# Kernel optimization log

Hardware: AMD Instinct MI355X
Metric: run time of the kernel (lower is better)

Reference implementation:

```python
import jax, jax.numpy as jnp
import numpy as np

N, E, F0, H = 100000, 3200000, 256, 128
TEMP = 2.0
ALPHA = 0.2  # leaky relu slope
EPS_BN = 1e-5
EPS_LN = 1e-5


def spmm(vals, row, col, X):
    # sparse [N,N] @ dense [N,D] via gather + segment_sum
    return jax.ops.segment_sum(vals[:, None] * X[col], row, num_segments=N)


def batchnorm(h, g, b):
    mu = jnp.mean(h, axis=0, keepdims=True)
    var = jnp.var(h, axis=0, keepdims=True)
    return (h - mu) * jax.lax.rsqrt(var + EPS_BN) * g + b


def layernorm(h, g, b):
    mu = jnp.mean(h, axis=-1, keepdims=True)
    var = jnp.var(h, axis=-1, keepdims=True)
    return (h - mu) * jax.lax.rsqrt(var + EPS_LN) * g + b


def setup_inputs() -> dict:
    key = jax.random.key(0)
    ks = jax.random.split(key, 32)
    x = jax.random.normal(ks[0], (N, F0), dtype=jnp.float32)
    edge_row = jax.random.randint(ks[1], (E,), 0, N)
    edge_col = jax.random.randint(ks[2], (E,), 0, N)
    adj_vals = jax.random.uniform(ks[3], (E,), dtype=jnp.float32) / 32.0  # ~normalized adj
    sf = lambda k, sh: jax.random.normal(k, sh, dtype=jnp.float32) * 0.05
    in_dim = 3 * F0 + 1
    return {
        "x": x, "edge_row": edge_row, "edge_col": edge_col, "adj_vals": adj_vals,
        # LowPassExtractor (GCN)
        "W_gc1": sf(ks[4], (F0, 2 * H)), "b_gc1": jnp.zeros((2 * H,), jnp.float32),
        "bn1_g": jnp.ones((2 * H,), jnp.float32), "bn1_b": jnp.zeros((2 * H,), jnp.float32),
        "W_gc2": sf(ks[5], (2 * H, H)), "b_gc2": jnp.zeros((H,), jnp.float32),
        "bn2_g": jnp.ones((H,), jnp.float32), "bn2_b": jnp.zeros((H,), jnp.float32),
        # Gating
        "Wg1": sf(ks[6], (in_dim, H)), "bg1": jnp.zeros((H,), jnp.float32),
        "ln_g": jnp.ones((H,), jnp.float32), "ln_b": jnp.zeros((H,), jnp.float32),
        "Wg2": sf(ks[7], (H, 2)), "bg2": jnp.zeros((2,), jnp.float32),
        # HighPassExpert
        "Wxp": sf(ks[8], (F0, H)), "bxp": jnp.zeros((H,), jnp.float32),
        "res_scale": jnp.asarray(1.0, jnp.float32),
        "rn_g": jnp.ones((H,), jnp.float32), "rn_b": jnp.zeros((H,), jnp.float32),
        "Wq": sf(ks[9], (H, H)), "Wk": sf(ks[10], (H, H)), "Wv": sf(ks[11], (H, H)),
    }


def reference(x, edge_row, edge_col, adj_vals,
              W_gc1, b_gc1, bn1_g, bn1_b, W_gc2, b_gc2, bn2_g, bn2_b,
              Wg1, bg1, ln_g, ln_b, Wg2, bg2,
              Wxp, bxp, res_scale, rn_g, rn_b, Wq, Wk, Wv):
    # ---- LowPassExtractor: two GCN layers (spmm(adj, xW)+b) with batchnorm+relu
    h1 = jax.nn.relu(batchnorm(spmm(adj_vals, edge_row, edge_col, x @ W_gc1) + b_gc1, bn1_g, bn1_b))
    low = jax.nn.relu(batchnorm(spmm(adj_vals, edge_row, edge_col, h1 @ W_gc2) + b_gc2, bn2_g, bn2_b))

    # ---- Gating: neighborhood stats via spmm
    AX = spmm(adj_vals, edge_row, edge_col, x)
    deg = jax.ops.segment_sum(adj_vals, edge_row, num_segments=N)[:, None]
    x_mean = AX / (deg + 1e-8)
    AX2 = spmm(adj_vals, edge_row, edge_col, x * x)
    var = AX2 / (deg + 1e-8) - x_mean * x_mean
    x_std = jnp.sqrt(jnp.clip(var, 0.0))
    x_cat = jnp.concatenate([x, AX - x, x_std, deg], axis=1)  # [N, 3*F0+1]
    hg = jax.nn.relu(layernorm(x_cat @ Wg1 + bg1, ln_g, ln_b))
    gate = jax.nn.softmax((hg @ Wg2 + bg2) / TEMP, axis=1)  # [N, 2]

    # ---- HighPassExpert: GAT-style sparse attention on normalized residual
    residual = layernorm(res_scale * (x @ Wxp + bxp - low), rn_g, rn_b)
    Q, K, V = residual @ Wq, residual @ Wk, residual @ Wv
    scores = jnp.sum(Q[edge_row] * K[edge_col], axis=1) / jnp.sqrt(jnp.float32(H))
    exp_s = jnp.exp(jnp.where(scores > 0, scores, ALPHA * scores))
    denom = jax.ops.segment_sum(exp_s, edge_row, num_segments=N)
    attn = exp_s / (denom[edge_row] + 1e-16)
    high = jax.ops.segment_sum(attn[:, None] * V[edge_col], edge_row, num_segments=N)

    output = gate[:, 0:1] * low + gate[:, 1:2] * high
    return output, gate, low, high
```

## Files before the change

kernel.cpp:

```cpp
#include <hip/hip_runtime.h>

#define F0 256
#define HD 128
#define NP 100352

typedef unsigned short u16;
typedef __attribute__((ext_vector_type(8))) short short8;
typedef __attribute__((ext_vector_type(4))) float f32x4;

__device__ inline float bf2f(u16 u) {
    union { unsigned int i; float f; } v; v.i = ((unsigned int)u) << 16; return v.f;
}
__device__ inline u16 f2bf(float f) {
    union { float f; unsigned int i; } v; v.f = f;
    unsigned int r = v.i + 0x7FFF + ((v.i >> 16) & 1);
    return (u16)(r >> 16);
}

#define GLOAD16(gp, lp) __builtin_amdgcn_global_load_lds( \
    (const __attribute__((address_space(1))) void*)(gp), \
    (__attribute__((address_space(3))) void*)(lp), 16, 0, 0)

__global__ void k_hist_rank(const int* __restrict__ row, int* __restrict__ counts,
                            int* __restrict__ rank, int E) {
    int e = blockIdx.x * blockDim.x + threadIdx.x;
    if (e < E) rank[e] = atomicAdd(&counts[row[e]], 1);
}

__global__ void k_scan_blk(const int* __restrict__ counts, int* __restrict__ scan_out,
                           int* __restrict__ partials, int n) {
    __shared__ int wsum[16];
    int t = threadIdx.x;
    int i = blockIdx.x * 1024 + t;
    int v = (i < n) ? counts[i] : 0;
    int lane = t & 63, w = t >> 6;
    #pragma unroll
    for (int off = 1; off < 64; off <<= 1) { int u = __shfl_up(v, off); if (lane >= off) v += u; }
    if (lane == 63) wsum[w] = v;
    __syncthreads();
    if (t < 16) {
        int s = wsum[t];
        #pragma unroll
        for (int off = 1; off < 16; off <<= 1) { int u = __shfl_up(s, off); if (t >= off) s += u; }
        wsum[t] = s;
    }
    __syncthreads();
    int add = (w > 0) ? wsum[w - 1] : 0;
    if (i < n) scan_out[i] = v + add;
    if (t == 1023) partials[blockIdx.x] = wsum[15];
}

__global__ void k_scan_part(int* partials, int nb) {
    __shared__ int ws2[2];
    int t = threadIdx.x;
    int v = (t < nb) ? partials[t] : 0;
    int lane = t & 63, w = t >> 6;
    #pragma unroll
    for (int off = 1; off < 64; off <<= 1) { int u = __shfl_up(v, off); if (lane >= off) v += u; }
    if (lane == 63) ws2[w] = v;
    __syncthreads();
    if (w == 1) v += ws2[0];
    if (t < nb) partials[t] = v;
}

__global__ void k_scan_add(int* __restrict__ row_ptr, const int* __restrict__ partials, int n) {
    int b = blockIdx.x;
    int i = b * 1024 + threadIdx.x;
    if (b == 0 && threadIdx.x == 0) row_ptr[0] = 0;
    int add = (b > 0) ? partials[b - 1] : 0;
    if (i < n) row_ptr[1 + i] += add;
}

__global__ void k_scatter_direct(const int* __restrict__ row, const int* __restrict__ ecol,
                                 const float* __restrict__ avals, const int* __restrict__ rank,
                                 const int* __restrict__ row_ptr, int2* __restrict__ cv, int E) {
    int e = blockIdx.x * blockDim.x + threadIdx.x;
    if (e >= E) return;
    int r = row[e];
    int pos = row_ptr[r] + rank[e];
    cv[pos] = make_int2(ecol[e], __float_as_int(avals[e]));
}

__global__ void k_cast_x(const float* __restrict__ x, u16* __restrict__ xb, int total4) {
    int i = blockIdx.x * blockDim.x + threadIdx.x;
    if (i >= total4) return;
    float4 v = ((const float4*)x)[i];
    ((ushort4*)xb)[i] = make_ushort4(f2bf(v.x), f2bf(v.y), f2bf(v.z), f2bf(v.w));
}

__global__ void k_prep_w(const float* __restrict__ W_gc1, const float* __restrict__ W_gc2,
                         const float* __restrict__ Wg1, const float* __restrict__ Wxp,
                         const float* __restrict__ Wq, const float* __restrict__ Wk,
                         const float* __restrict__ Wv,
                         u16* Wgc1t, u16* Wgc2t, u16* Wdt, u16* W1t, u16* W2t,
                         u16* Wxpt, u16* Wqt, u16* Wkt, u16* Wvt) {
    int z = blockIdx.z;
    int idx = blockIdx.x * 256 + threadIdx.x;
    if (z == 0) { if (idx < 65536) { int n = idx >> 8, k = idx & 255; Wgc1t[idx] = f2bf(W_gc1[k * 256 + n]); } }
    else if (z == 1) { if (idx < 32768) { int n = idx >> 8, k = idx & 255; Wgc2t[idx] = f2bf(W_gc2[k * 128 + n]); } }
    else if (z == 2) { if (idx < 32768) { int n = idx >> 8, k = idx & 255; Wdt[idx] = f2bf(Wg1[k * 128 + n] - Wg1[(k + 256) * 128 + n]); } }
    else if (z == 3) { if (idx < 32768) { int n = idx >> 8, k = idx & 255; W1t[idx] = f2bf(Wg1[(k + 256) * 128 + n]); } }
    else if (z == 4) { if (idx < 32768) { int n = idx >> 8, k = idx & 255; W2t[idx] = f2bf(Wg1[(k + 512) * 128 + n]); } }
    else if (z == 5) { if (idx < 32768) { int n = idx >> 8, k = idx & 255; Wxpt[idx] = f2bf(Wxp[k * 128 + n]); } }
    else if (z == 6) { if (idx < 16384) { int n = idx >> 7, k = idx & 127; Wqt[idx] = f2bf(Wq[k * 128 + n]); } }
    else if (z == 7) { if (idx < 16384) { int n = idx >> 7, k = idx & 127; Wkt[idx] = f2bf(Wk[k * 128 + n]); } }
    else if (z == 8) { if (idx < 16384) { int n = idx >> 7, k = idx & 127; Wvt[idx] = f2bf(Wv[k * 128 + n]); } }
}

__global__ void k_spmm_x2(const u16* __restrict__ Xb, const int* __restrict__ row_ptr,
                          const int2* __restrict__ cv,
                          u16* __restrict__ AXb, u16* __restrict__ XSTDb,
                          float* __restrict__ deg, int N) {
    int wid = blockIdx.x * 4 + (threadIdx.x >> 6);
    if (wid >= N) return;
    int lane = threadIdx.x & 63;
    float a0 = 0, a1 = 0, a2 = 0, a3 = 0;
    float q0 = 0, q1 = 0, q2 = 0, q3 = 0, d = 0;
    int s = row_ptr[wid], e = row_ptr[wid + 1];
    int j = s;
    for (; j + 7 < e; j += 8) {
        int2 cc[8]; ushort4 xb[8];
        #pragma unroll
        for (int t = 0; t < 8; ++t) cc[t] = cv[j + t];
        #pragma unroll
        for (int t = 0; t < 8; ++t) xb[t] = *(const ushort4*)(Xb + (size_t)cc[t].x * F0 + lane * 4);
        #pragma unroll
        for (int t = 0; t < 8; ++t) {
            float x0 = bf2f(xb[t].x), x1 = bf2f(xb[t].y), x2 = bf2f(xb[t].z), x3 = bf2f(xb[t].w);
            float vv = __int_as_float(cc[t].y);
            a0 += vv * x0; a1 += vv * x1; a2 += vv * x2; a3 += vv * x3;
            q0 += vv * x0 * x0; q1 += vv * x1 * x1; q2 += vv * x2 * x2; q3 += vv * x3 * x3;
            d += vv;
        }
    }
    for (; j + 3 < e; j += 4) {
        int2 cc[4]; ushort4 xb[4];
        #pragma unroll
        for (int t = 0; t < 4; ++t) cc[t] = cv[j + t];
        #pragma unroll
        for (int t = 0; t < 4; ++t) xb[t] = *(const ushort4*)(Xb + (size_t)cc[t].x * F0 + lane * 4);
        #pragma unroll
        for (int t = 0; t < 4; ++t) {
            float x0 = bf2f(xb[t].x), x1 = bf2f(xb[t].y), x2 = bf2f(xb[t].z), x3 = bf2f(xb[t].w);
            float vv = __int_as_float(cc[t].y);
            a0 += vv * x0; a1 += vv * x1; a2 += vv * x2; a3 += vv * x3;
            q0 += vv * x0 * x0; q1 += vv * x1 * x1; q2 += vv * x2 * x2; q3 += vv * x3 * x3;
            d += vv;
        }
    }
    for (; j < e; ++j) {
        int2 cc = cv[j];
        float v0 = __int_as_float(cc.y);
        ushort4 xb0 = *(const ushort4*)(Xb + (size_t)cc.x * F0 + lane * 4);
        float x0 = bf2f(xb0.x), x1 = bf2f(xb0.y), x2 = bf2f(xb0.z), x3 = bf2f(xb0.w);
        a0 += v0 * x0; a1 += v0 * x1; a2 += v0 * x2; a3 += v0 * x3;
        q0 += v0 * x0 * x0; q1 += v0 * x1 * x1; q2 += v0 * x2 * x2; q3 += v0 * x3 * x3;
        d += v0;
    }
    float inv = 1.0f / (d + 1e-8f);
    float m0 = a0 * inv, m1 = a1 * inv, m2 = a2 * inv, m3 = a3 * inv;
    float s0 = sqrtf(fmaxf(q0 * inv - m0 * m0, 0.f));
    float s1 = sqrtf(fmaxf(q1 * inv - m1 * m1, 0.f));
    float s2 = sqrtf(fmaxf(q2 * inv - m2 * m2, 0.f));
    float s3 = sqrtf(fmaxf(q3 * inv - m3 * m3, 0.f));
    *(ushort4*)(AXb + (size_t)wid * F0 + lane * 4) = make_ushort4(f2bf(a0), f2bf(a1), f2bf(a2), f2bf(a3));
    *(ushort4*)(XSTDb + (size_t)wid * F0 + lane * 4) = make_ushort4(f2bf(s0), f2bf(s1), f2bf(s2), f2bf(s3));
    if (lane == 0) deg[wid] = d;
}

__global__ void k_spmm128(const u16* __restrict__ Xb, const int* __restrict__ row_ptr,
                          const int2* __restrict__ cv, u16* __restrict__ OUT, int N) {
    int wid = blockIdx.x * 4 + (threadIdx.x >> 6);
    if (wid >= N) return;
    int lane = threadIdx.x & 63;
    float a0 = 0, a1 = 0;
    int s = row_ptr[wid], e = row_ptr[wid + 1];
    int j = s;
    for (; j + 7 < e; j += 8) {
        int2 cc[8]; ushort2 xb[8];
        #pragma unroll
        for (int t = 0; t < 8; ++t) cc[t] = cv[j + t];
        #pragma unroll
        for (int t = 0; t < 8; ++t) xb[t] = *(const ushort2*)(Xb + (size_t)cc[t].x * HD + lane * 2);
        #pragma unroll
        for (int t = 0; t < 8; ++t) {
            float vv = __int_as_float(cc[t].y);
            a0 += vv * bf2f(xb[t].x); a1 += vv * bf2f(xb[t].y);
        }
    }
    for (; j + 3 < e; j += 4) {
        int2 cc[4]; ushort2 xb[4];
        #pragma unroll
        for (int t = 0; t < 4; ++t) cc[t] = cv[j + t];
        #pragma unroll
        for (int t = 0; t < 4; ++t) xb[t] = *(const ushort2*)(Xb + (size_t)cc[t].x * HD + lane * 2);
        #pragma unroll
        for (int t = 0; t < 4; ++t) {
            float vv = __int_as_float(cc[t].y);
            a0 += vv * bf2f(xb[t].x); a1 += vv * bf2f(xb[t].y);
        }
    }
    for (; j < e; ++j) {
        int2 cc = cv[j];
        float v0 = __int_as_float(cc.y);
        ushort2 x0 = *(const ushort2*)(Xb + (size_t)cc.x * HD + lane * 2);
        a0 += v0 * bf2f(x0.x); a1 += v0 * bf2f(x0.y);
    }
    *(ushort2*)(OUT + (size_t)wid * HD + lane * 2) = make_ushort2(f2bf(a0), f2bf(a1));
}

__device__ inline void mm_core(const u16* __restrict__ A, const u16* __restrict__ Bt,
                               int K, int ldA, int ldB, int m0, int n0,
                               u16* As, u16* Bs, f32x4 acc[4][4]) {
    int t = threadIdx.x, w = t >> 6, l = t & 63;
    int wr = (w >> 1) * 64, wc = (w & 1) * 64;
    int aoff = (wr + (l & 15)) * 32 + (l >> 4) * 8;
    int boff = (wc + (l & 15)) * 32 + (l >> 4) * 8;
    for (int k0 = 0; k0 < K; k0 += 32) {
        __syncthreads();
        #pragma unroll
        for (int s = 0; s < 2; ++s) {
            int i = s * 256 + t;
            int row = i >> 2, ch = i & 3;
            GLOAD16(A + (size_t)(m0 + row) * ldA + k0 + ch * 8, As + i * 8);
            GLOAD16(Bt + (size_t)(n0 + row) * ldB + k0 + ch * 8, Bs + i * 8);
        }
        __syncthreads();
        short8 af[4], bfr[4];
        #pragma unroll
        for (int i = 0; i < 4; ++i) af[i] = *(const short8*)(As + aoff + i * 16 * 32);
        #pragma unroll
        for (int j = 0; j < 4; ++j) bfr[j] = *(const short8*)(Bs + boff + j * 16 * 32);
        #pragma unroll
        for (int i = 0; i < 4; ++i)
            #pragma unroll
            for (int j = 0; j < 4; ++j)
                acc[i][j] = __builtin_amdgcn_mfma_f32_16x16x32_bf16(af[i], bfr[j], acc[i][j], 0, 0, 0);
    }
}

__device__ inline void mm_zero(f32x4 acc[4][4]) {
    #pragma unroll
    for (int i = 0; i < 4; ++i)
        #pragma unroll
        for (int j = 0; j < 4; ++j)
            acc[i][j] = (f32x4){0.f, 0.f, 0.f, 0.f};
}

__global__ __launch_bounds__(256) void k_mm_f32(const u16* __restrict__ A, const u16* __restrict__ Bt,
                                                float* __restrict__ C, const float* __restrict__ bias,
                                                int M, int K, int Nc) {
    __shared__ __align__(16) u16 As[128 * 32];
    __shared__ __align__(16) u16 Bs[128 * 32];
    int m0 = blockIdx.x * 128, n0 = blockIdx.y * 128;
    f32x4 acc[4][4]; mm_zero(acc);
    mm_core(A, Bt, K, K, K, m0, n0, As, Bs, acc);
    int t = threadIdx.x, w = t >> 6, l = t & 63;
    int rbase = m0 + (w >> 1) * 64 + (l >> 4) * 4;
    int cbase = n0 + (w & 1) * 64 + (l & 15);
    #pragma unroll
    for (int j = 0; j < 4; ++j) {
        float bj = bias ? bias[cbase + j * 16] : 0.f;
        #pragma unroll
        for (int i = 0; i < 4; ++i)
            #pragma unroll
            for (int r = 0; r < 4; ++r) {
                int row = rbase + i * 16 + r;
                if (row < M) C[(size_t)row * Nc + cbase + j * 16] = acc[i][j][r] + bj;
            }
    }
}

__global__ __launch_bounds__(256) void k_mm_bf(const u16* __restrict__ A, const u16* __restrict__ Bt,
                                               u16* __restrict__ C, int M, int K, int Nc) {
    __shared__ __align__(16) u16 As[128 * 32];
    __shared__ __align__(16) u16 Bs[128 * 32];
    int m0 = blockIdx.x * 128, n0 = blockIdx.y * 128;
    f32x4 acc[4][4]; mm_zero(acc);
    mm_core(A, Bt, K, K, K, m0, n0, As, Bs, acc);
    int t = threadIdx.x, w = t >> 6, l = t & 63;
    int rbase = m0 + (w >> 1) * 64 + (l >> 4) * 4;
    int cbase = n0 + (w & 1) * 64 + (l & 15);
    #pragma unroll
    for (int j = 0; j < 4; ++j)
        #pragma unroll
        for (int i = 0; i < 4; ++i)
            #pragma unroll
            for (int r = 0; r < 4; ++r) {
                int row = rbase + i * 16 + r;
                if (row < M) C[(size_t)row * Nc + cbase + j * 16] = f2bf(acc[i][j][r]);
            }
}

__global__ __launch_bounds__(256) void k_mm_gate(const u16* A0, const u16* A1, const u16* A2,
                                                 const u16* B0, const u16* B1, const u16* B2,
                                                 float* __restrict__ C, const float* __restrict__ bg1,
                                                 const float* __restrict__ wlast,
                                                 const float* __restrict__ deg, int M) {
    __shared__ __align__(16) u16 As[128 * 32];
    __shared__ __align__(16) u16 Bs[128 * 32];
    int m0 = blockIdx.x * 128;
    f32x4 acc[4][4]; mm_zero(acc);
    mm_core(A0, B0, 256, 256, 256, m0, 0, As, Bs, acc);
    mm_core(A1, B1, 256, 256, 256, m0, 0, As, Bs, acc);
    mm_core(A2, B2, 256, 256, 256, m0, 0, As, Bs, acc);
    int t = threadIdx.x, w = t >> 6, l = t & 63;
    int rbase = m0 + (w >> 1) * 64 + (l >> 4) * 4;
    int cbase = (w & 1) * 64 + (l & 15);
    float wl[4], bg[4];
    #pragma unroll
    for (int j = 0; j < 4; ++j) { wl[j] = wlast[cbase + j * 16]; bg[j] = bg1[cbase + j * 16]; }
    float dg[4][4];
    #pragma unroll
    for (int i = 0; i < 4; ++i)
        #pragma unroll
        for (int r = 0; r < 4; ++r) {
            int row = rbase + i * 16 + r;
            dg[i][r] = (row < M) ? deg[row] : 0.f;
        }
    #pragma unroll
    for (int j = 0; j < 4; ++j)
        #pragma unroll
        for (int i = 0; i < 4; ++i)
            #pragma unroll
            for (int r = 0; r < 4; ++r) {
                int row = rbase + i * 16 + r;
                if (row < M) C[(size_t)row * 128 + cbase + j * 16] = acc[i][j][r] + bg[j] + dg[i][r] * wl[j];
            }
}

__global__ __launch_bounds__(256) void k_mm_qkv(const u16* __restrict__ A,
                                                const u16* Wqt, const u16* Wkt, const u16* Wvt,
                                                float* Q, u16* KV, int M) {
    __shared__ __align__(16) u16 As[128 * 32];
    __shared__ __align__(16) u16 Bs[128 * 32];
    int z = blockIdx.z;
    const u16* Bt = (z == 0) ? Wqt : (z == 1) ? Wkt : Wvt;
    int m0 = blockIdx.x * 128;
    f32x4 acc[4][4]; mm_zero(acc);
    mm_core(A, Bt, 128, 128, 128, m0, 0, As, Bs, acc);
    int t = threadIdx.x, w = t >> 6, l = t & 63;
    int rbase = m0 + (w >> 1) * 64 + (l >> 4) * 4;
    int cbase = (w & 1) * 64 + (l & 15);
    if (z == 0) {
        #pragma unroll
        for (int j = 0; j < 4; ++j)
            #pragma unroll
            for (int i = 0; i < 4; ++i)
                #pragma unroll
                for (int r = 0; r < 4; ++r) {
                    int row = rbase + i * 16 + r;
                    if (row < M) Q[(size_t)row * 128 + cbase + j * 16] = acc[i][j][r];
                }
    } else {
        int coff = (z == 1) ? 0 : 128;
        #pragma unroll
        for (int j = 0; j < 4; ++j)
            #pragma unroll
            for (int i = 0; i < 4; ++i)
                #pragma unroll
                for (int r = 0; r < 4; ++r) {
                    int row = rbase + i * 16 + r;
                    if (row < M) KV[(size_t)row * 256 + coff + cbase + j * 16] = f2bf(acc[i][j][r]);
                }
    }
}

__global__ void k_bn_stats_bf(const u16* __restrict__ H, double* __restrict__ stats, int N, int C) {
    int t = threadIdx.x;
    int rpt = 256 / C;
    int rsub = t / C;
    int col = t - rsub * C;
    double s = 0.0, q = 0.0;
    for (long r = (long)blockIdx.x * rpt + rsub; r < N; r += (long)gridDim.x * rpt) {
        float v = bf2f(H[(size_t)r * C + col]);
        s += v; q += (double)v * v;
    }
    __shared__ double sh_s[256], sh_q[256];
    sh_s[t] = s; sh_q[t] = q;
    __syncthreads();
    if (t < C) {
        for (int k = 1; k < rpt; ++k) { s += sh_s[t + k * C]; q += sh_q[t + k * C]; }
        atomicAdd(&stats[t], s);
        atomicAdd(&stats[C + t], q);
    }
}

__global__ void k_bn_fin(const double* __restrict__ stats, const float* __restrict__ g,
                         const float* __restrict__ b, float* __restrict__ scale,
                         float* __restrict__ shift, int C, double invN) {
    int t = threadIdx.x;
    if (t >= C) return;
    double mean = stats[t] * invN;
    double var = stats[C + t] * invN - mean * mean;
    float sc = (float)((double)g[t] / sqrt(var + 1e-5));
    scale[t] = sc;
    shift[t] = b[t] - (float)mean * sc;
}

__global__ void k_bn_relu_bb(const u16* __restrict__ in, u16* __restrict__ out,
                             const float* __restrict__ scale, const float* __restrict__ shift,
                             int total4, int cmask4) {
    int i = blockIdx.x * blockDim.x + threadIdx.x;
    if (i >= total4) return;
    int c4 = i & cmask4;
    ushort4 v = ((const ushort4*)in)[i];
    float4 sc = ((const float4*)scale)[c4];
    float4 sh = ((const float4*)shift)[c4];
    ((ushort4*)out)[i] = make_ushort4(
        f2bf(fmaxf(bf2f(v.x) * sc.x + sh.x, 0.f)), f2bf(fmaxf(bf2f(v.y) * sc.y + sh.y, 0.f)),
        f2bf(fmaxf(bf2f(v.z) * sc.z + sh.z, 0.f)), f2bf(fmaxf(bf2f(v.w) * sc.w + sh.w, 0.f)));
}

__global__ void k_bn_relu_bf(const u16* __restrict__ in, float* __restrict__ out,
                             const float* __restrict__ scale, const float* __restrict__ shift,
                             int total4, int cmask4) {
    int i = blockIdx.x * blockDim.x + threadIdx.x;
    if (i >= total4) return;
    int c4 = i & cmask4;
    ushort4 v = ((const ushort4*)in)[i];
    float4 sc = ((const float4*)scale)[c4];
    float4 sh = ((const float4*)shift)[c4];
    ((float4*)out)[i] = make_float4(
        fmaxf(bf2f(v.x) * sc.x + sh.x, 0.f), fmaxf(bf2f(v.y) * sc.y + sh.y, 0.f),
        fmaxf(bf2f(v.z) * sc.z + sh.z, 0.f), fmaxf(bf2f(v.w) * sc.w + sh.w, 0.f));
}

__global__ void k_ln_gate(const float* __restrict__ Hg, const float* __restrict__ g,
                          const float* __restrict__ b, const float* __restrict__ Wg2,
                          const float* __restrict__ bg2, float* __restrict__ gate, int N) {
    int wid = blockIdx.x * 4 + (threadIdx.x >> 6);
    if (wid >= N) return;
    int lane = threadIdx.x & 63;
    float2 h = *(const float2*)(Hg + (size_t)wid * HD + lane * 2);
    float s1 = h.x + h.y, s2 = h.x * h.x + h.y * h.y;
    #pragma unroll
    for (int off = 32; off > 0; off >>= 1) { s1 += __shfl_xor(s1, off); s2 += __shfl_xor(s2, off); }
    float mu = s1 * (1.f / 128.f);
    float var = s2 * (1.f / 128.f) - mu * mu;
    float is = 1.0f / sqrtf(var + 1e-5f);
    float2 gg = *(const float2*)(g + lane * 2);
    float2 bb = *(const float2*)(b + lane * 2);
    float y0 = fmaxf((h.x - mu) * is * gg.x + bb.x, 0.f);
    float y1 = fmaxf((h.y - mu) * is * gg.y + bb.y, 0.f);
    float4 w = ((const float4*)Wg2)[lane];
    float t0 = y0 * w.x + y1 * w.z;
    float t1 = y0 * w.y + y1 * w.w;
    #pragma unroll
    for (int off = 32; off > 0; off >>= 1) { t0 += __shfl_xor(t0, off); t1 += __shfl_xor(t1, off); }
    if (lane == 0) {
        t0 = (t0 + bg2[0]) * 0.5f;
        t1 = (t1 + bg2[1]) * 0.5f;
        float m = fmaxf(t0, t1);
        float e0 = __expf(t0 - m), e1 = __expf(t1 - m);
        float inv = 1.0f / (e0 + e1);
        gate[(size_t)wid * 2 + 0] = e0 * inv;
        gate[(size_t)wid * 2 + 1] = e1 * inv;
    }
}

__global__ void k_resid_ln(const float* __restrict__ R0, const float* __restrict__ low,
                           const float* __restrict__ g, const float* __restrict__ b,
                           const float* __restrict__ rs_ptr, u16* __restrict__ resid, int N) {
    int wid = blockIdx.x * 4 + (threadIdx.x >> 6);
    if (wid >= N) return;
    int lane = threadIdx.x & 63;
    float rs = rs_ptr[0];
    float2 a = *(const float2*)(R0 + (size_t)wid * HD + lane * 2);
    float2 l = *(const float2*)(low + (size_t)wid * HD + lane * 2);
    float h0 = rs * (a.x - l.x), h1 = rs * (a.y - l.y);
    float s1 = h0 + h1, s2 = h0 * h0 + h1 * h1;
    #pragma unroll
    for (int off = 32; off > 0; off >>= 1) { s1 += __shfl_xor(s1, off); s2 += __shfl_xor(s2, off); }
    float mu = s1 * (1.f / 128.f);
    float var = s2 * (1.f / 128.f) - mu * mu;
    float is = 1.0f / sqrtf(var + 1e-5f);
    float2 gg = *(const float2*)(g + lane * 2);
    float2 bb = *(const float2*)(b + lane * 2);
    float y0 = (h0 - mu) * is * gg.x + bb.x;
    float y1 = (h1 - mu) * is * gg.y + bb.y;
    *(ushort2*)(resid + (size_t)wid * HD + lane * 2) = make_ushort2(f2bf(y0), f2bf(y1));
}

__global__ void k_attn_aggr(const float* __restrict__ Q, const u16* __restrict__ KV,
                            const int* __restrict__ row_ptr, const int2* __restrict__ cv,
                            const float* __restrict__ gate, const float* __restrict__ low,
                            float* __restrict__ high, float* __restrict__ outp, int N) {
    int wid = blockIdx.x * 4 + (threadIdx.x >> 6);
    if (wid >= N) return;
    int lane = threadIdx.x & 63;
    int sub = lane & 15;
    int g = lane >> 4;
    float qs[8];
    {
        const float4* qp = (const float4*)(Q + (size_t)wid * HD + sub * 8);
        float4 q0 = qp[0], q1 = qp[1];
        qs[0] = q0.x; qs[1] = q0.y; qs[2] = q0.z; qs[3] = q0.w;
        qs[4] = q1.x; qs[5] = q1.y; qs[6] = q1.z; qs[7] = q1.w;
    }
    float2 qv = *(const float2*)(Q + (size_t)wid * HD + lane * 2);
    float n0 = 0, n1 = 0, den = 0;
    int s = row_ptr[wid], e = row_ptr[wid + 1];
    int j = s;
    for (; j + 7 < e; j += 8) {
        int cg0 = cv[j + g].x;
        int cg1 = cv[j + 4 + g].x;
        short8 ka = *(const short8*)(KV + (size_t)cg0 * 256 + sub * 8);
        short8 kb = *(const short8*)(KV + (size_t)cg1 * 256 + sub * 8);
        float p0 = qs[0] * bf2f((u16)ka[0]) + qs[1] * bf2f((u16)ka[1])
                 + qs[2] * bf2f((u16)ka[2]) + qs[3] * bf2f((u16)ka[3])
                 + qs[4] * bf2f((u16)ka[4]) + qs[5] * bf2f((u16)ka[5])
                 + qs[6] * bf2f((u16)ka[6]) + qs[7] * bf2f((u16)ka[7]);
        float p1 = qs[0] * bf2f((u16)kb[0]) + qs[1] * bf2f((u16)kb[1])
                 + qs[2] * bf2f((u16)kb[2]) + qs[3] * bf2f((u16)kb[3])
                 + qs[4] * bf2f((u16)kb[4]) + qs[5] * bf2f((u16)kb[5])
                 + qs[6] * bf2f((u16)kb[6]) + qs[7] * bf2f((u16)kb[7]);
        p0 += __shfl_xor(p0, 1); p1 += __shfl_xor(p1, 1);
        p0 += __shfl_xor(p0, 2); p1 += __shfl_xor(p1, 2);
        p0 += __shfl_xor(p0, 4); p1 += __shfl_xor(p1, 4);
        p0 += __shfl_xor(p0, 8); p1 += __shfl_xor(p1, 8);
        float sc0 = p0 * 0.08838834764831845f;
        float sc1 = p1 * 0.08838834764831845f;
        float ls0 = sc0 > 0.f ? sc0 : 0.2f * sc0;
        float ls1 = sc1 > 0.f ? sc1 : 0.2f * sc1;
        float ex0 = __expf(ls0);
        float ex1 = __expf(ls1);
        float exb[8]; int cb[8];
        #pragma unroll
        for (int t = 0; t < 4; ++t) {
            exb[t]     = __shfl(ex0, t << 4); cb[t]     = __shfl(cg0, t << 4);
            exb[4 + t] = __shfl(ex1, t << 4); cb[4 + t] = __shfl(cg1, t << 4);
        }
        ushort2 vb[8];
        #pragma unroll
        for (int t = 0; t < 8; ++t) vb[t] = *(const ushort2*)(KV + (size_t)cb[t] * 256 + 128 + lane * 2);
        #pragma unroll
        for (int t = 0; t < 8; ++t) {
            n0 += exb[t] * bf2f(vb[t].x);
            n1 += exb[t] * bf2f(vb[t].y);
            den += exb[t];
        }
    }
    for (; j + 3 < e; j += 4) {
        int cg = cv[j + g].x;
        short8 kk = *(const short8*)(KV + (size_t)cg * 256 + sub * 8);
        float p = qs[0] * bf2f((u16)kk[0]) + qs[1] * bf2f((u16)kk[1])
                + qs[2] * bf2f((u16)kk[2]) + qs[3] * bf2f((u16)kk[3])
                + qs[4] * bf2f((u16)kk[4]) + qs[5] * bf2f((u16)kk[5])
                + qs[6] * bf2f((u16)kk[6]) + qs[7] * bf2f((u16)kk[7]);
        p += __shfl_xor(p, 1); p += __shfl_xor(p, 2);
        p += __shfl_xor(p, 4); p += __shfl_xor(p, 8);
        float sc = p * 0.08838834764831845f;
        float ls = sc > 0.f ? sc : 0.2f * sc;
        float ex = __expf(ls);
        float exb[4]; int cb[4];
        #pragma unroll
        for (int t = 0; t < 4; ++t) { exb[t] = __shfl(ex, t << 4); cb[t] = __shfl(cg, t << 4); }
        ushort2 vb[4];
        #pragma unroll
        for (int t = 0; t < 4; ++t) vb[t] = *(const ushort2*)(KV + (size_t)cb[t] * 256 + 128 + lane * 2);
        #pragma unroll
        for (int t = 0; t < 4; ++t) {
            n0 += exb[t] * bf2f(vb[t].x);
            n1 += exb[t] * bf2f(vb[t].y);
            den += exb[t];
        }
    }
    for (; j < e; ++j) {
        int c0 = cv[j].x;
        ushort2 kb0 = *(const ushort2*)(KV + (size_t)c0 * 256 + lane * 2);
        ushort2 vb0 = *(const ushort2*)(KV + (size_t)c0 * 256 + 128 + lane * 2);
        float sc0 = qv.x * bf2f(kb0.x) + qv.y * bf2f(kb0.y);
        #pragma unroll
        for (int off = 32; off > 0; off >>= 1) sc0 += __shfl_xor(sc0, off);
        float p = sc0 * 0.08838834764831845f;
        float ls = p > 0.f ? p : 0.2f * p;
        float ex = __expf(ls);
        n0 += ex * bf2f(vb0.x); n1 += ex * bf2f(vb0.y); den += ex;
    }
    float inv = 1.0f / (den + 1e-16f);
    float h0 = n0 * inv, h1 = n1 * inv;
    *(float2*)(high + (size_t)wid * HD + lane * 2) = make_float2(h0, h1);
    float g0 = gate[(size_t)wid * 2 + 0], g1 = gate[(size_t)wid * 2 + 1];
    float2 lw = *(const float2*)(low + (size_t)wid * HD + lane * 2);
    *(float2*)(outp + (size_t)wid * HD + lane * 2) = make_float2(g0 * lw.x + g1 * h0, g0 * lw.y + g1 * h1);
}

extern "C" void kernel_launch(void* const* d_in, const int* in_sizes, int n_in,
                              void* d_out, int out_size, void* d_ws, size_t ws_size,
                              hipStream_t stream) {
    const float* x      = (const float*)d_in[0];
    const int*   erow   = (const int*)d_in[1];
    const int*   ecol   = (const int*)d_in[2];
    const float* avals  = (const float*)d_in[3];
    const float* W_gc1  = (const float*)d_in[4];
    const float* bn1_g  = (const float*)d_in[6];
    const float* bn1_b  = (const float*)d_in[7];
    const float* W_gc2  = (const float*)d_in[8];
    const float* bn2_g  = (const float*)d_in[10];
    const float* bn2_b  = (const float*)d_in[11];
    const float* Wg1    = (const float*)d_in[12];
    const float* bg1    = (const float*)d_in[13];
    const float* ln_g   = (const float*)d_in[14];
    const float* ln_b   = (const float*)d_in[15];
    const float* Wg2    = (const float*)d_in[16];
    const float* bg2    = (const float*)d_in[17];
    const float* Wxp    = (const float*)d_in[18];
    const float* bxp    = (const float*)d_in[19];
    const float* rscale = (const float*)d_in[20];
    const float* rn_g   = (const float*)d_in[21];
    const float* rn_b   = (const float*)d_in[22];
    const float* Wq     = (const float*)d_in[23];
    const float* Wk     = (const float*)d_in[24];
    const float* Wv     = (const float*)d_in[25];

    const int N = in_sizes[0] / F0;
    const int E = in_sizes[1];

    char* base = (char*)d_ws;
    size_t off = 0;
    auto carve = [&](size_t bytes) -> char* {
        char* p = base + off;
        off += (bytes + 255) & ~(size_t)255;
        return p;
    };
    double* stats  = (double*)carve(4096);
    float* scaleb  = (float*)carve(1024);
    float* shiftb  = (float*)carve(1024);
    int*   partials= (int*)carve(2048);
    u16* Wgc1t = (u16*)carve(65536 * 2);
    u16* Wgc2t = (u16*)carve(32768 * 2);
    u16* Wdt   = (u16*)carve(32768 * 2);
    u16* W1t   = (u16*)carve(32768 * 2);
    u16* W2t   = (u16*)carve(32768 * 2);
    u16* Wxpt  = (u16*)carve(32768 * 2);
    u16* Wqt   = (u16*)carve(16384 * 2);
    u16* Wkt   = (u16*)carve(16384 * 2);
    u16* Wvt   = (u16*)carve(16384 * 2);
    int*   row_ptr = (int*)carve((size_t)(N + 1) * 4);
    int*   cursor  = (int*)carve((size_t)N * 4);
    float* deg     = (float*)carve((size_t)N * 4);
    int2*  cv      = (int2*)carve((size_t)E * 8);
    u16*   x_bf    = (u16*)carve((size_t)NP * F0 * 2);
    u16*   kvb     = (u16*)carve((size_t)NP * 256 * 2);
    u16*   AX_bf   = (u16*)carve((size_t)NP * F0 * 2);
    u16*   XSTD_bf = (u16*)carve((size_t)NP * F0 * 2);
    u16*   h1_bf   = (u16*)carve((size_t)NP * F0 * 2);
    float* BIG3    = (float*)carve((size_t)NP * HD * 4);
    u16*   G2_bf   = (u16*)carve((size_t)NP * HD * 2);
    float* M3      = (float*)carve((size_t)NP * HD * 4);
    (void)ws_size; (void)n_in; (void)out_size;

    u16*   S1_bf = h1_bf;
    u16*   S2_bf = (u16*)BIG3;
    u16*   resid_bf = h1_bf;
    int*   rank  = (int*)M3;

    float* out_o    = (float*)d_out;
    float* out_gate = out_o + (size_t)N * HD;
    float* out_low  = out_gate + (size_t)N * 2;
    float* out_high = out_low + (size_t)N * HD;

    const int eb  = (E + 255) / 256;
    const int wb  = (N + 3) / 4;
    const int NB1 = (N + 1023) / 1024;
    const int gx  = (N + 127) / 128;
    const dim3 blk(256);

    hipMemsetAsync(cursor, 0, (size_t)N * 4, stream);
    k_hist_rank<<<eb, blk, 0, stream>>>(erow, cursor, rank, E);
    k_scan_blk<<<NB1, 1024, 0, stream>>>(cursor, row_ptr + 1, partials, N);
    k_scan_part<<<1, 128, 0, stream>>>(partials, NB1);
    k_scan_add<<<NB1, 1024, 0, stream>>>(row_ptr, partials, N);
    k_scatter_direct<<<eb, blk, 0, stream>>>(erow, ecol, avals, rank, row_ptr, cv, E);

    k_cast_x<<<(N * 64 + 255) / 256, blk, 0, stream>>>(x, x_bf, N * 64);
    k_prep_w<<<dim3(256, 1, 9), blk, 0, stream>>>(W_gc1, W_gc2, Wg1, Wxp, Wq, Wk, Wv,
                                                  Wgc1t, Wgc2t, Wdt, W1t, W2t, Wxpt, Wqt, Wkt, Wvt);

    k_spmm_x2<<<wb, blk, 0, stream>>>(x_bf, row_ptr, cv, AX_bf, XSTD_bf, deg, N);

    k_mm_bf<<<dim3(gx, 2), blk, 0, stream>>>(AX_bf, Wgc1t, S1_bf, N, 256, 256);
    hipMemsetAsync(stats, 0, 4096, stream);
    k_bn_stats_bf<<<1024, blk, 0, stream>>>(S1_bf, stats, N, 256);
    k_bn_fin<<<1, blk, 0, stream>>>(stats, bn1_g, bn1_b, scaleb, shiftb, 256, 1.0 / N);
    k_bn_relu_bb<<<(N * 64 + 255) / 256, blk, 0, stream>>>(S1_bf, h1_bf, scaleb, shiftb, N * 64, 63);
    k_mm_bf<<<dim3(gx, 1), blk, 0, stream>>>(h1_bf, Wgc2t, G2_bf, N, 256, 128);
    k_spmm128<<<wb, blk, 0, stream>>>(G2_bf, row_ptr, cv, S2_bf, N);
    hipMemsetAsync(stats, 0, 2048, stream);
    k_bn_stats_bf<<<1024, blk, 0, stream>>>(S2_bf, stats, N, 128);
    k_bn_fin<<<1, blk, 0, stream>>>(stats, bn2_g, bn2_b, scaleb, shiftb, 128, 1.0 / N);
    k_bn_relu_bf<<<(N * 32 + 255) / 256, blk, 0, stream>>>(S2_bf, out_low, scaleb, shiftb, N * 32, 31);

    k_mm_gate<<<dim3(gx, 1), blk, 0, stream>>>(x_bf, AX_bf, XSTD_bf, Wdt, W1t, W2t,
                                               M3, bg1, Wg1 + (size_t)768 * 128, deg, N);
    k_ln_gate<<<wb, blk, 0, stream>>>(M3, ln_g, ln_b, Wg2, bg2, out_gate, N);

    k_mm_f32<<<dim3(gx, 1), blk, 0, stream>>>(x_bf, Wxpt, BIG3, bxp, N, 256, 128);
    k_resid_ln<<<wb, blk, 0, stream>>>(BIG3, out_low, rn_g, rn_b, rscale, resid_bf, N);
    k_mm_qkv<<<dim3(gx, 1, 3), blk, 0, stream>>>(resid_bf, Wqt, Wkt, Wvt, M3, kvb, N);
    k_attn_aggr<<<wb, blk, 0, stream>>>(M3, kvb, row_ptr, cv, out_gate, out_low, out_high, out_o, N);
}
```

Before: 1.458 ms.

## Fuse layernorm epilogues into gate and residual GEMMs, store Q in bf16

The gating GEMM now computes bias, layernorm, ReLU, the 2-way projection and the softmax in its epilogue, using cross-lane shuffles and shared-memory partial sums across the two column-half waves. The Wxp GEMM likewise fuses the residual subtraction and layernorm and writes bf16 directly. Together these drop two separate kernels and two fp32 N×128 intermediate round-trips. Q is also stored as bf16 to halve its traffic in the attention kernel, at some cost in precision.

```diff
diff --git a/kernel.cpp b/kernel.cpp
--- a/kernel.cpp
+++ b/kernel.cpp
@@ -15,6 +15,12 @@
     union { float f; unsigned int i; } v; v.f = f;
     unsigned int r = v.i + 0x7FFF + ((v.i >> 16) & 1);
     return (u16)(r >> 16);
+}
+
+__device__ inline float rsum16(float v) {
+    v += __shfl_xor(v, 1); v += __shfl_xor(v, 2);
+    v += __shfl_xor(v, 4); v += __shfl_xor(v, 8);
+    return v;
 }
 
 #define GLOAD16(gp, lp) __builtin_amdgcn_global_load_lds( \
@@ -247,30 +253,6 @@
             acc[i][j] = (f32x4){0.f, 0.f, 0.f, 0.f};
 }
 
-__global__ __launch_bounds__(256) void k_mm_f32(const u16* __restrict__ A, const u16* __restrict__ Bt,
-                                                float* __restrict__ C, const float* __restrict__ bias,
-                                                int M, int K, int Nc) {
-    __shared__ __align__(16) u16 As[128 * 32];
-    __shared__ __align__(16) u16 Bs[128 * 32];
-    int m0 = blockIdx.x * 128, n0 = blockIdx.y * 128;
-    f32x4 acc[4][4]; mm_zero(acc);
-    mm_core(A, Bt, K, K, K, m0, n0, As, Bs, acc);
-    int t = threadIdx.x, w = t >> 6, l = t & 63;
-    int rbase = m0 + (w >> 1) * 64 + (l >> 4) * 4;
-    int cbase = n0 + (w & 1) * 64 + (l & 15);
-    #pragma unroll
-    for (int j = 0; j < 4; ++j) {
-        float bj = bias ? bias[cbase + j * 16] : 0.f;
-        #pragma unroll
-        for (int i = 0; i < 4; ++i)
-            #pragma unroll
-            for (int r = 0; r < 4; ++r) {
-                int row = rbase + i * 16 + r;
-                if (row < M) C[(size_t)row * Nc + cbase + j * 16] = acc[i][j][r] + bj;
-            }
-    }
-}
-
 __global__ __launch_bounds__(256) void k_mm_bf(const u16* __restrict__ A, const u16* __restrict__ Bt,
                                                u16* __restrict__ C, int M, int K, int Nc) {
     __shared__ __align__(16) u16 As[128 * 32];
@@ -294,44 +276,156 @@
 
 __global__ __launch_bounds__(256) void k_mm_gate(const u16* A0, const u16* A1, const u16* A2,
                                                  const u16* B0, const u16* B1, const u16* B2,
-                                                 float* __restrict__ C, const float* __restrict__ bg1,
+                                                 const float* __restrict__ bg1,
                                                  const float* __restrict__ wlast,
-                                                 const float* __restrict__ deg, int M) {
+                                                 const float* __restrict__ deg,
+                                                 const float* __restrict__ ln_g,
+                                                 const float* __restrict__ ln_b,
+                                                 const float* __restrict__ Wg2,
+                                                 const float* __restrict__ bg2,
+                                                 float* __restrict__ gate, int M) {
     __shared__ __align__(16) u16 As[128 * 32];
     __shared__ __align__(16) u16 Bs[128 * 32];
+    __shared__ float ps1[2][128], ps2[2][128], pt0[2][128], pt1[2][128];
     int m0 = blockIdx.x * 128;
     f32x4 acc[4][4]; mm_zero(acc);
     mm_core(A0, B0, 256, 256, 256, m0, 0, As, Bs, acc);
     mm_core(A1, B1, 256, 256, 256, m0, 0, As, Bs, acc);
     mm_core(A2, B2, 256, 256, 256, m0, 0, As, Bs, acc);
     int t = threadIdx.x, w = t >> 6, l = t & 63;
-    int rbase = m0 + (w >> 1) * 64 + (l >> 4) * 4;
-    int cbase = (w & 1) * 64 + (l & 15);
-    float wl[4], bg[4];
-    #pragma unroll
-    for (int j = 0; j < 4; ++j) { wl[j] = wlast[cbase + j * 16]; bg[j] = bg1[cbase + j * 16]; }
-    float dg[4][4];
+    int hcol = w & 1;
+    int lr0 = (w >> 1) * 64 + (l >> 4) * 4;
+    int cbase = hcol * 64 + (l & 15);
+    float wl[4], bg[4], lg[4], lb[4], wa[4], wb_[4];
+    #pragma unroll
+    for (int j = 0; j < 4; ++j) {
+        int col = cbase + j * 16;
+        wl[j] = wlast[col]; bg[j] = bg1[col];
+        lg[j] = ln_g[col];  lb[j] = ln_b[col];
+        wa[j] = Wg2[col * 2 + 0]; wb_[j] = Wg2[col * 2 + 1];
+    }
     #pragma unroll
     for (int i = 0; i < 4; ++i)
         #pragma unroll
         for (int r = 0; r < 4; ++r) {
-            int row = rbase + i * 16 + r;
-            dg[i][r] = (row < M) ? deg[row] : 0.f;
-        }
-    #pragma unroll
-    for (int j = 0; j < 4; ++j)
+            int row = m0 + lr0 + i * 16 + r;
+            float dgv = (row < M) ? deg[row] : 0.f;
+            float s1 = 0.f, s2 = 0.f;
+            #pragma unroll
+            for (int j = 0; j < 4; ++j) {
+                float h = acc[i][j][r] + bg[j] + dgv * wl[j];
+                acc[i][j][r] = h;
+                s1 += h; s2 += h * h;
+            }
+            s1 = rsum16(s1); s2 = rsum16(s2);
+            if ((l & 15) == 0) { ps1[hcol][lr0 + i * 16 + r] = s1; ps2[hcol][lr0 + i * 16 + r] = s2; }
+        }
+    __syncthreads();
+    #pragma unroll
+    for (int i = 0; i < 4; ++i)
+        #pragma unroll
+        for (int r = 0; r < 4; ++r) {
+            int lr = lr0 + i * 16 + r;
+            float s1 = ps1[0][lr] + ps1[1][lr];
+            float s2 = ps2[0][lr] + ps2[1][lr];
+            float mu = s1 * (1.f / 128.f);
+            float var = s2 * (1.f / 128.f) - mu * mu;
+            float is = 1.0f / sqrtf(var + 1e-5f);
+            float t0 = 0.f, t1 = 0.f;
+            #pragma unroll
+            for (int j = 0; j < 4; ++j) {
+                float y = fmaxf((acc[i][j][r] - mu) * is * lg[j] + lb[j], 0.f);
+                t0 += y * wa[j]; t1 += y * wb_[j];
+            }
+            t0 = rsum16(t0); t1 = rsum16(t1);
+            if ((l & 15) == 0) { pt0[hcol][lr] = t0; pt1[hcol][lr] = t1; }
+        }
+    __syncthreads();
+    if (hcol == 0 && (l & 15) == 0) {
+        float b20 = bg2[0], b21 = bg2[1];
         #pragma unroll
         for (int i = 0; i < 4; ++i)
             #pragma unroll
             for (int r = 0; r < 4; ++r) {
-                int row = rbase + i * 16 + r;
-                if (row < M) C[(size_t)row * 128 + cbase + j * 16] = acc[i][j][r] + bg[j] + dg[i][r] * wl[j];
+                int lr = lr0 + i * 16 + r;
+                int row = m0 + lr;
+                if (row >= M) continue;
+                float t0 = (pt0[0][lr] + pt0[1][lr] + b20) * 0.5f;
+                float t1 = (pt1[0][lr] + pt1[1][lr] + b21) * 0.5f;
+                float m = fmaxf(t0, t1);
+                float e0 = __expf(t0 - m), e1 = __expf(t1 - m);
+                float inv = 1.0f / (e0 + e1);
+                gate[(size_t)row * 2 + 0] = e0 * inv;
+                gate[(size_t)row * 2 + 1] = e1 * inv;
             }
+    }
+}
+
+__global__ __launch_bounds__(256) void k_mm_xp(const u16* __restrict__ A, const u16* __restrict__ Bt,
+                                               const float* __restrict__ bias,
+                                               const float* __restrict__ low,
+                                               const float* __restrict__ g,
+                                               const float* __restrict__ b,
+                                               const float* __restrict__ rs_ptr,
+                                               u16* __restrict__ resid, int M) {
+    __shared__ __align__(16) u16 As[128 * 32];
+    __shared__ __align__(16) u16 Bs[128 * 32];
+    __shared__ float ps1[2][128], ps2[2][128];
+    int m0 = blockIdx.x * 128;
+    f32x4 acc[4][4]; mm_zero(acc);
+    mm_core(A, Bt, 256, 256, 256, m0, 0, As, Bs, acc);
+    int t = threadIdx.x, w = t >> 6, l = t & 63;
+    int hcol = w & 1;
+    int lr0 = (w >> 1) * 64 + (l >> 4) * 4;
+    int cbase = hcol * 64 + (l & 15);
+    float rs = rs_ptr[0];
+    float bx[4], lg[4], lb[4];
+    #pragma unroll
+    for (int j = 0; j < 4; ++j) {
+        int col = cbase + j * 16;
+        bx[j] = bias[col]; lg[j] = g[col]; lb[j] = b[col];
+    }
+    #pragma unroll
+    for (int i = 0; i < 4; ++i)
+        #pragma unroll
+        for (int r = 0; r < 4; ++r) {
+            int row = m0 + lr0 + i * 16 + r;
+            float s1 = 0.f, s2 = 0.f;
+            #pragma unroll
+            for (int j = 0; j < 4; ++j) {
+                float lv = (row < M) ? low[(size_t)row * 128 + cbase + j * 16] : 0.f;
+                float h = rs * (acc[i][j][r] + bx[j] - lv);
+                acc[i][j][r] = h;
+                s1 += h; s2 += h * h;
+            }
+            s1 = rsum16(s1); s2 = rsum16(s2);
+            if ((l & 15) == 0) { ps1[hcol][lr0 + i * 16 + r] = s1; ps2[hcol][lr0 + i * 16 + r] = s2; }
+        }
+    __syncthreads();
+    #pragma unroll
+    for (int i = 0; i < 4; ++i)
+        #pragma unroll
+        for (int r = 0; r < 4; ++r) {
+            int lr = lr0 + i * 16 + r;
+            int row = m0 + lr;
+            float s1 = ps1[0][lr] + ps1[1][lr];
+            float s2 = ps2[0][lr] + ps2[1][lr];
+            float mu = s1 * (1.f / 128.f);
+            float var = s2 * (1.f / 128.f) - mu * mu;
+            float is = 1.0f / sqrtf(var + 1e-5f);
+            if (row < M) {
+                #pragma unroll
+                for (int j = 0; j < 4; ++j) {
+                    float y = (acc[i][j][r] - mu) * is * lg[j] + lb[j];
+                    resid[(size_t)row * 128 + cbase + j * 16] = f2bf(y);
+                }
+            }
+        }
 }
 
 __global__ __launch_bounds__(256) void k_mm_qkv(const u16* __restrict__ A,
                                                 const u16* Wqt, const u16* Wkt, const u16* Wvt,
-                                                float* Q, u16* KV, int M) {
+                                                u16* Qb, u16* KV, int M) {
     __shared__ __align__(16) u16 As[128 * 32];
     __shared__ __align__(16) u16 Bs[128 * 32];
     int z = blockIdx.z;
@@ -350,7 +444,7 @@
                 #pragma unroll
                 for (int r = 0; r < 4; ++r) {
                     int row = rbase + i * 16 + r;
-                    if (row < M) Q[(size_t)row * 128 + cbase + j * 16] = acc[i][j][r];
+                    if (row < M) Qb[(size_t)row * 128 + cbase + j * 16] = f2bf(acc[i][j][r]);
                 }
     } else {
         int coff = (z == 1) ? 0 : 128;
@@ -426,63 +520,7 @@
         fmaxf(bf2f(v.z) * sc.z + sh.z, 0.f), fmaxf(bf2f(v.w) * sc.w + sh.w, 0.f));
 }
 
-__global__ void k_ln_gate(const float* __restrict__ Hg, const float* __restrict__ g,
-                          const float* __restrict__ b, const float* __restrict__ Wg2,
-                          const float* __restrict__ bg2, float* __restrict__ gate, int N) {
-    int wid = blockIdx.x * 4 + (threadIdx.x >> 6);
-    if (wid >= N) return;
-    int lane = threadIdx.x & 63;
-    float2 h = *(const float2*)(Hg + (size_t)wid * HD + lane * 2);
-    float s1 = h.x + h.y, s2 = h.x * h.x + h.y * h.y;
-    #pragma unroll
-    for (int off = 32; off > 0; off >>= 1) { s1 += __shfl_xor(s1, off); s2 += __shfl_xor(s2, off); }
-    float mu = s1 * (1.f / 128.f);
-    float var = s2 * (1.f / 128.f) - mu * mu;
-    float is = 1.0f / sqrtf(var + 1e-5f);
-    float2 gg = *(const float2*)(g + lane * 2);
-    float2 bb = *(const float2*)(b + lane * 2);
-    float y0 = fmaxf((h.x - mu) * is * gg.x + bb.x, 0.f);
-    float y1 = fmaxf((h.y - mu) * is * gg.y + bb.y, 0.f);
-    float4 w = ((const float4*)Wg2)[lane];
-    float t0 = y0 * w.x + y1 * w.z;
-    float t1 = y0 * w.y + y1 * w.w;
-    #pragma unroll
-    for (int off = 32; off > 0; off >>= 1) { t0 += __shfl_xor(t0, off); t1 += __shfl_xor(t1, off); }
-    if (lane == 0) {
-        t0 = (t0 + bg2[0]) * 0.5f;
-        t1 = (t1 + bg2[1]) * 0.5f;
-        float m = fmaxf(t0, t1);
-        float e0 = __expf(t0 - m), e1 = __expf(t1 - m);
-        float inv = 1.0f / (e0 + e1);
-        gate[(size_t)wid * 2 + 0] = e0 * inv;
-        gate[(size_t)wid * 2 + 1] = e1 * inv;
-    }
-}
-
-__global__ void k_resid_ln(const float* __restrict__ R0, const float* __restrict__ low,
-                           const float* __restrict__ g, const float* __restrict__ b,
-                           const float* __restrict__ rs_ptr, u16* __restrict__ resid, int N) {
-    int wid = blockIdx.x * 4 + (threadIdx.x >> 6);
-    if (wid >= N) return;
-    int lane = threadIdx.x & 63;
-    float rs = rs_ptr[0];
-    float2 a = *(const float2*)(R0 + (size_t)wid * HD + lane * 2);
-    float2 l = *(const float2*)(low + (size_t)wid * HD + lane * 2);
-    float h0 = rs * (a.x - l.x), h1 = rs * (a.y - l.y);
-    float s1 = h0 + h1, s2 = h0 * h0 + h1 * h1;
-    #pragma unroll
-    for (int off = 32; off > 0; off >>= 1) { s1 += __shfl_xor(s1, off); s2 += __shfl_xor(s2, off); }
-    float mu = s1 * (1.f / 128.f);
-    float var = s2 * (1.f / 128.f) - mu * mu;
-    float is = 1.0f / sqrtf(var + 1e-5f);
-    float2 gg = *(const float2*)(g + lane * 2);
-    float2 bb = *(const float2*)(b + lane * 2);
-    float y0 = (h0 - mu) * is * gg.x + bb.x;
-    float y1 = (h1 - mu) * is * gg.y + bb.y;
-    *(ushort2*)(resid + (size_t)wid * HD + lane * 2) = make_ushort2(f2bf(y0), f2bf(y1));
-}
-
-__global__ void k_attn_aggr(const float* __restrict__ Q, const u16* __restrict__ KV,
+__global__ void k_attn_aggr(const u16* __restrict__ Qb, const u16* __restrict__ KV,
                             const int* __restrict__ row_ptr, const int2* __restrict__ cv,
                             const float* __restrict__ gate, const float* __restrict__ low,
                             float* __restrict__ high, float* __restrict__ outp, int N) {
@@ -493,12 +531,15 @@
     int g = lane >> 4;
     float qs[8];
     {
-        const float4* qp = (const float4*)(Q + (size_t)wid * HD + sub * 8);
-        float4 q0 = qp[0], q1 = qp[1];
-        qs[0] = q0.x; qs[1] = q0.y; qs[2] = q0.z; qs[3] = q0.w;
-        qs[4] = q1.x; qs[5] = q1.y; qs[6] = q1.z; qs[7] = q1.w;
-    }
-    float2 qv = *(const float2*)(Q + (size_t)wid * HD + lane * 2);
+        short8 q8 = *(const short8*)(Qb + (size_t)wid * HD + sub * 8);
+        #pragma unroll
+        for (int k = 0; k < 8; ++k) qs[k] = bf2f((u16)q8[k]);
+    }
+    float2 qv;
+    {
+        ushort2 qt = *(const ushort2*)(Qb + (size_t)wid * HD + lane * 2);
+        qv.x = bf2f(qt.x); qv.y = bf2f(qt.y);
+    }
     float n0 = 0, n1 = 0, den = 0;
     int s = row_ptr[wid], e = row_ptr[wid + 1];
     int j = s;
@@ -646,15 +687,15 @@
     u16*   AX_bf   = (u16*)carve((size_t)NP * F0 * 2);
     u16*   XSTD_bf = (u16*)carve((size_t)NP * F0 * 2);
     u16*   h1_bf   = (u16*)carve((size_t)NP * F0 * 2);
-    float* BIG3    = (float*)carve((size_t)NP * HD * 4);
+    u16*   S2_bf   = (u16*)carve((size_t)NP * HD * 2);
     u16*   G2_bf   = (u16*)carve((size_t)NP * HD * 2);
     float* M3      = (float*)carve((size_t)NP * HD * 4);
     (void)ws_size; (void)n_in; (void)out_size;
 
     u16*   S1_bf = h1_bf;
-    u16*   S2_bf = (u16*)BIG3;
     u16*   resid_bf = h1_bf;
     int*   rank  = (int*)M3;
+    u16*   Qb    = (u16*)M3;
 
     float* out_o    = (float*)d_out;
     float* out_gate = out_o + (size_t)N * HD;
@@ -693,11 +734,11 @@
     k_bn_relu_bf<<<(N * 32 + 255) / 256, blk, 0, stream>>>(S2_bf, out_low, scaleb, shiftb, N * 32, 31);
 
     k_mm_gate<<<dim3(gx, 1), blk, 0, stream>>>(x_bf, AX_bf, XSTD_bf, Wdt, W1t, W2t,
-                                               M3, bg1, Wg1 + (size_t)768 * 128, deg, N);
-    k_ln_gate<<<wb, blk, 0, stream>>>(M3, ln_g, ln_b, Wg2, bg2, out_gate, N);
-
-    k_mm_f32<<<dim3(gx, 1), blk, 0, stream>>>(x_bf, Wxpt, BIG3, bxp, N, 256, 128);
-    k_resid_ln<<<wb, blk, 0, stream>>>(BIG3, out_low, rn_g, rn_b, rscale, resid_bf, N);
-    k_mm_qkv<<<dim3(gx, 1, 3), blk, 0, stream>>>(resid_bf, Wqt, Wkt, Wvt, M3, kvb, N);
-    k_attn_aggr<<<wb, blk, 0, stream>>>(M3, kvb, row_ptr, cv, out_gate, out_low, out_high, out_o, N);
-}
+                                               bg1, Wg1 + (size_t)768 * 128, deg,
+                                               ln_g, ln_b, Wg2, bg2, out_gate, N);
+
+    k_mm_xp<<<dim3(gx, 1), blk, 0, stream>>>(x_bf, Wxpt, bxp, out_low, rn_g, rn_b, rscale,
+                                             resid_bf, N);
+    k_mm_qkv<<<dim3(gx, 1, 3), blk, 0, stream>>>(resid_bf, Wqt, Wkt, Wvt, Qb, kvb, N);
+    k_attn_aggr<<<wb, blk, 0, stream>>>(Qb, kvb, row_ptr, cv, out_gate, out_low, out_high, out_o, N);
+}
```

Measured after the change: 1.410 ms. -3.3%, faster.
